# Kernel tuning notes

Measured on AMD Instinct MI355X. Metric: run time of the kernel, lower is better.

Reference implementation:

```python
import jax, jax.numpy as jnp
import numpy as np

NS, NV = 48, 10            # scalar / vector multiplicities
IN_SIZE = NS + 3*NV + 3*NV + NS   # 156
N_EDGE_FEAT = 96
HIDDEN = 96
# weight shapes per output irrep: 0e:(58,48) 1o:(68,10) 1e:(68,10) 0o:(58,48)
W_SHAPES = [('0e', NS + NV, NS), ('1o', NS + 2*NV, NV), ('1e', 2*NV + NS, NV), ('0o', NV + NS, NS)]
WEIGHT_NUMEL = sum(a*b for _, a, b in W_SHAPES)  # 6928
N_NODES, N_EDGES = 10000, 50000


def setup_inputs() -> dict:
    key = jax.random.key(0)
    ks = jax.random.split(key, 9)
    node_attr = jax.random.normal(ks[0], (N_NODES, IN_SIZE), dtype=jnp.float32)
    edge_index = jax.random.randint(ks[1], (2, N_EDGES), 0, N_NODES)
    edge_attr = jax.random.normal(ks[2], (N_EDGES, N_EDGE_FEAT), dtype=jnp.float32)
    edge_sh = jax.random.normal(ks[3], (N_EDGES, 4), dtype=jnp.float32)
    s1 = 1.0 / np.sqrt(N_EDGE_FEAT)
    s2 = 1.0 / np.sqrt(HIDDEN)
    W1 = jax.random.normal(ks[4], (N_EDGE_FEAT, HIDDEN), dtype=jnp.float32) * s1
    b1 = jnp.zeros((HIDDEN,), dtype=jnp.float32)
    W2 = jax.random.normal(ks[5], (HIDDEN, WEIGHT_NUMEL), dtype=jnp.float32) * s2
    b2 = jnp.zeros((WEIGHT_NUMEL,), dtype=jnp.float32)
    return {'node_attr': node_attr, 'edge_index': edge_index, 'edge_attr': edge_attr,
            'edge_sh': edge_sh, 'W1': W1, 'b1': b1, 'W2': W2, 'b2': b2}


def _faster_tp(in_, sh, weight):
    # in_: [E, 156], sh: [E, 4], weight: [E, 6928]
    in_0e = in_[:, :NS]                                   # [E,48]
    in_1o = in_[:, NS:NS + 3*NV].reshape(-1, NV, 3)       # [E,10,3]
    in_1e = in_[:, NS + 3*NV:NS + 6*NV].reshape(-1, NV, 3)
    in_0o = in_[:, NS + 6*NV:]                            # [E,48]
    sh_0e = sh[:, 0]                                      # [E]
    sh_1o = sh[:, 1:]                                     # [E,3]
    inv_s3 = 1.0 / np.sqrt(3.0)
    inv_s2 = 1.0 / np.sqrt(2.0)

    out_0e = jnp.concatenate([
        in_0e * sh_0e[:, None],
        jnp.sum(in_1o * sh_1o[:, None, :], axis=-1) * inv_s3], axis=-1)      # [E,58]
    out_1o = jnp.concatenate([
        in_0e[:, :, None] * sh_1o[:, None, :],
        in_1o * sh_0e[:, None, None],
        jnp.cross(in_1e, sh_1o[:, None, :]) * inv_s2], axis=-2)              # [E,68,3]
    out_1e = jnp.concatenate([
        jnp.cross(in_1o, sh_1o[:, None, :]) * inv_s2,
        in_1e * sh_0e[:, None, None],
        in_0o[:, :, None] * sh_1o[:, None, :]], axis=-2)                     # [E,68,3]
    out_0o = jnp.concatenate([
        jnp.sum(in_1e * sh_1o[:, None, :], axis=-1) * inv_s3,
        in_0o * sh_0e[:, None]], axis=-1)                                    # [E,58]

    wd = {}
    start = 0
    for name, a, b in W_SHAPES:
        wd[name] = weight[:, start:start + a*b].reshape(-1, a, b) / np.sqrt(a)
        start += a*b

    o0e = jnp.einsum('ei,eio->eo', out_0e, wd['0e'])                 # [E,48]
    o1o = jnp.einsum('eic,eio->eoc', out_1o, wd['1o']).reshape(-1, 3*NV)
    o1e = jnp.einsum('eic,eio->eoc', out_1e, wd['1e']).reshape(-1, 3*NV)
    o0o = jnp.einsum('ei,eio->eo', out_0o, wd['0o'])                 # [E,48]
    return jnp.concatenate([o0e, o1o, o1e, o0o], axis=-1)           # [E,156]


def reference(node_attr, edge_index, edge_attr, edge_sh, W1, b1, W2, b2):
    edge_src, edge_dst = edge_index[0], edge_index[1]
    # edge MLP -> per-edge TP weights
    h = jax.nn.relu(edge_attr @ W1 + b1)
    w = h @ W2 + b2                                       # [E, 6928]
    tp = _faster_tp(node_attr[edge_dst], edge_sh, w)      # [E, 156]
    # scatter-mean over source nodes
    n = node_attr.shape[0]
    seg = jax.ops.segment_sum(tp, edge_src, num_segments=n)
    cnt = jax.ops.segment_sum(jnp.ones((tp.shape[0],), tp.dtype), edge_src, num_segments=n)
    out = seg / jnp.maximum(cnt, 1.0)[:, None]
    # residual (in/out sizes equal, so pad is a no-op)
    return out + node_attr
```

## Files before the change

kernel.cpp:

```cpp
#include <hip/hip_runtime.h>

#define NE 50000
#define NN 10000
#define KH 96
#define KE 128
#define WN 6928
#define WP 7744
#define NTILE 484
#define IN_SZ 156
#define EPW 32

typedef __attribute__((ext_vector_type(8))) short short8;
typedef __attribute__((ext_vector_type(4))) float float4v;

__device__ __forceinline__ unsigned short f2bf(float x) {
  unsigned u = __float_as_uint(x);
  unsigned r = (u + 0x7FFFu + ((u >> 16) & 1u)) >> 16;
  return (unsigned short)r;
}
__device__ __forceinline__ float b2f(unsigned short u) {
  return __uint_as_float(((unsigned)u) << 16);
}

__device__ __forceinline__ void issue4(short8 (&B)[4], const unsigned short* p) {
  asm volatile("global_load_dwordx4 %0, %4, off\n\t"
               "global_load_dwordx4 %1, %4, off offset:1024\n\t"
               "global_load_dwordx4 %2, %4, off offset:2048\n\t"
               "global_load_dwordx4 %3, %4, off offset:3072"
               : "=&v"(B[0]), "=&v"(B[1]), "=&v"(B[2]), "=&v"(B[3])
               : "v"(p));
}
__device__ __forceinline__ void wait4(short8 (&B)[4]) {
  asm volatile("s_waitcnt vmcnt(4)"
               : "+v"(B[0]), "+v"(B[1]), "+v"(B[2]), "+v"(B[3]));
}
__device__ __forceinline__ void wait0(short8 (&B)[4]) {
  asm volatile("s_waitcnt vmcnt(0)"
               : "+v"(B[0]), "+v"(B[1]), "+v"(B[2]), "+v"(B[3]));
}

__global__ __launch_bounds__(256) void cast_kernel(
    const float* __restrict__ edge_attr, const float* __restrict__ W1,
    unsigned short* __restrict__ ea_bf, unsigned short* __restrict__ W1T)
{
  int idx = blockIdx.x * 256 + threadIdx.x;
  const int nea = NE * KH / 8;
  if (idx < nea) {
    const float* p = edge_attr + (size_t)idx * 8;
    float4 x = *(const float4*)p, y = *(const float4*)(p + 4);
    uint4 pk;
    pk.x = f2bf(x.x) | ((unsigned)f2bf(x.y) << 16);
    pk.y = f2bf(x.z) | ((unsigned)f2bf(x.w) << 16);
    pk.z = f2bf(y.x) | ((unsigned)f2bf(y.y) << 16);
    pk.w = f2bf(y.z) | ((unsigned)f2bf(y.w) << 16);
    *(uint4*)(ea_bf + (size_t)idx * 8) = pk;
  } else {
    int j = idx - nea;
    if (j < KH * KH) {
      int c = j / KH, k = j - c * KH;
      W1T[c * KH + k] = f2bf(W1[k * KH + c]);
    }
  }
}

__global__ __launch_bounds__(384) void mlp1_kernel(
    const unsigned short* __restrict__ ea_bf, const unsigned short* __restrict__ W1T,
    const float* __restrict__ b1, unsigned short* __restrict__ h_ext)
{
  const int tid = threadIdx.x;
  const int e0 = blockIdx.x * 16;
  const int w = tid >> 6, l = tid & 15, q = (tid >> 4) & 3;

  short8 a[3], b[3];
  #pragma unroll
  for (int s = 0; s < 3; ++s) {
    a[s] = *(const short8*)(ea_bf + (size_t)(e0 + l) * KH + s * 32 + q * 8);
    b[s] = *(const short8*)(W1T + (size_t)(w * 16 + l) * KH + s * 32 + q * 8);
  }
  float4v C = {0.f, 0.f, 0.f, 0.f};
  #pragma unroll
  for (int s = 0; s < 3; ++s)
    C = __builtin_amdgcn_mfma_f32_16x16x32_bf16(a[s], b[s], C, 0, 0, 0);

  float bv = b1[w * 16 + l];
  #pragma unroll
  for (int r = 0; r < 4; ++r)
    h_ext[(size_t)(e0 + q * 4 + r) * KE + w * 16 + l] = f2bf(fmaxf(C[r] + bv, 0.f));

  for (int idx = tid; idx < 16 * 32; idx += 384) {
    int e = idx >> 5, c = 96 + (idx & 31);
    h_ext[(size_t)(e0 + e) * KE + c] = (c == 96) ? (unsigned short)0x3F80 : (unsigned short)0;
  }
}

__global__ __launch_bounds__(256) void w2pt_kernel(
    const float* __restrict__ W2, const float* __restrict__ b2,
    unsigned short* __restrict__ W2PT)
{
  int gid = blockIdx.x * 256 + threadIdx.x;
  if (gid >= NTILE * 256) return;
  int lane = gid & 63, s = (gid >> 6) & 3, t = gid >> 8;
  int l = lane & 15, q = lane >> 4;
  int np = t * 16 + l;
  int c;
  if (np < 2784) c = np;
  else if (np < 3872) { int rel = np - 2784, i = rel >> 4, o = rel & 15; c = (o < 10) ? 2784 + i * 10 + o : -1; }
  else if (np < 4960) { int rel = np - 3872, i = rel >> 4, o = rel & 15; c = (o < 10) ? 3464 + i * 10 + o : -1; }
  else c = 4144 + (np - 4960);

  int kbase = s * 32 + q * 8;
  unsigned short o8[8];
  #pragma unroll
  for (int j = 0; j < 8; ++j) {
    int k = kbase + j;
    float v = 0.f;
    if (c >= 0) v = (k < KH) ? W2[(size_t)k * WN + c] : (k == KH ? b2[c] : 0.f);
    o8[j] = f2bf(v);
  }
  uint4 pk;
  pk.x = o8[0] | ((unsigned)o8[1] << 16);
  pk.y = o8[2] | ((unsigned)o8[3] << 16);
  pk.z = o8[4] | ((unsigned)o8[5] << 16);
  pk.w = o8[6] | ((unsigned)o8[7] << 16);
  *(uint4*)(W2PT + (size_t)gid * 8) = pk;
}

__global__ __launch_bounds__(512, 2) void tp_kernel(
    const unsigned short* __restrict__ h_ext, const float* __restrict__ node_attr,
    const int* __restrict__ edge_index, const float* __restrict__ edge_sh,
    const unsigned short* __restrict__ W2PT,
    float* __restrict__ acc, int* __restrict__ icnt)
{
  __shared__ unsigned short sIn[EPW][160];
  __shared__ float sOut[EPW][160];
  __shared__ unsigned short sF0[2][60][EPW];
  __shared__ unsigned short sF1[2][70][3][EPW];
  __shared__ float sShs[EPW][4];
  __shared__ int sSrc[EPW], sDst[EPW];

  const int tid = threadIdx.x;
  const int e0 = blockIdx.x * EPW;

  if (tid < EPW) {
    int ok = (e0 + tid) < NE;
    int s = ok ? edge_index[e0 + tid] : 0;
    int d = ok ? edge_index[NE + e0 + tid] : 0;
    sSrc[tid] = s; sDst[tid] = d;
    if (ok) atomicAdd(&icnt[s], 1);
  }
  if (tid >= 128 && tid < 256) {
    int t2 = tid - 128;
    int e = t2 >> 2, c = t2 & 3;
    sShs[e][c] = ((e0 + e) < NE) ? edge_sh[(size_t)(e0 + e) * 4 + c] : 0.f;
  }
  __syncthreads();

  for (int idx = tid; idx < EPW * IN_SZ; idx += 512) {
    int e = idx / IN_SZ, f = idx - e * IN_SZ;
    sIn[e][f] = f2bf(node_attr[(size_t)sDst[e] * IN_SZ + f]);
  }
  for (int idx = tid; idx < EPW * 160; idx += 512) (&sOut[0][0])[idx] = 0.f;
  __syncthreads();

  {
    const int e = tid >> 4, j = tid & 15;
    const float sh0 = sShs[e][0], sx = sShs[e][1], sy = sShs[e][2], sz = sShs[e][3];
    const float i3 = 0.57735026918962576f, i2 = 0.70710678118654752f;
    for (int i = j; i < 48; i += 16) {
      float v0 = b2f(sIn[e][i]), w0 = b2f(sIn[e][108 + i]);
      sF0[0][i][e] = f2bf(v0 * sh0);
      sF0[1][10 + i][e] = f2bf(w0 * sh0);
      sF1[0][i][0][e] = f2bf(v0 * sx); sF1[0][i][1][e] = f2bf(v0 * sy); sF1[0][i][2][e] = f2bf(v0 * sz);
      sF1[1][20 + i][0][e] = f2bf(w0 * sx); sF1[1][20 + i][1][e] = f2bf(w0 * sy); sF1[1][20 + i][2][e] = f2bf(w0 * sz);
    }
    if (j < 10) {
      const int v = j;
      float ax = b2f(sIn[e][48 + 3 * v]), ay = b2f(sIn[e][48 + 3 * v + 1]), az = b2f(sIn[e][48 + 3 * v + 2]);
      float bx = b2f(sIn[e][78 + 3 * v]), by = b2f(sIn[e][78 + 3 * v + 1]), bz = b2f(sIn[e][78 + 3 * v + 2]);
      sF0[0][48 + v][e] = f2bf((ax * sx + ay * sy + az * sz) * i3);
      sF0[1][v][e]      = f2bf((bx * sx + by * sy + bz * sz) * i3);
      sF1[0][48 + v][0][e] = f2bf(ax * sh0); sF1[0][48 + v][1][e] = f2bf(ay * sh0); sF1[0][48 + v][2][e] = f2bf(az * sh0);
      sF1[0][58 + v][0][e] = f2bf((by * sz - bz * sy) * i2);
      sF1[0][58 + v][1][e] = f2bf((bz * sx - bx * sz) * i2);
      sF1[0][58 + v][2][e] = f2bf((bx * sy - by * sx) * i2);
      sF1[1][v][0][e] = f2bf((ay * sz - az * sy) * i2);
      sF1[1][v][1][e] = f2bf((az * sx - ax * sz) * i2);
      sF1[1][v][2][e] = f2bf((ax * sy - ay * sx) * i2);
      sF1[1][10 + v][0][e] = f2bf(bx * sh0); sF1[1][10 + v][1][e] = f2bf(by * sh0); sF1[1][10 + v][2][e] = f2bf(bz * sh0);
    }
  }
  if (tid < 128) {
    int fam = tid >> 6, i = 58 + ((tid >> 5) & 1), e = tid & 31;
    sF0[fam][i][e] = 0;
  } else if (tid < 128 + 384) {
    int t2 = tid - 128;
    int fam = t2 / 192, r = t2 - fam * 192;
    int i = 68 + (r / 96), r2 = r % 96, cc = r2 >> 5, e = r2 & 31;
    sF1[fam][i][cc][e] = 0;
  }
  __syncthreads();

  const int wv = tid >> 6, l = tid & 15, q = (tid >> 4) & 3;

  short8 Af[2][4];
  #pragma unroll
  for (int m = 0; m < 2; ++m) {
    const unsigned short* ar = h_ext + (size_t)(e0 + m * 16 + l) * KE + q * 8;
    #pragma unroll
    for (int s = 0; s < 4; ++s) Af[m][s] = *(const short8*)(ar + s * 32);
  }

  const unsigned short* wlane = W2PT + (size_t)(tid & 63) * 8;
  short8 Ba[4], Bb[4];

  if (wv < 4) {
    const int sf = wv >> 1;
    const int ibeg = (wv & 1) * 30;
    const int tb = sf ? 310 : 0;
    const int obase = sf ? 108 : 0;
    #pragma unroll 1
    for (int ob = 0; ob < 3; ++ob) {
      float a0[4] = {0.f, 0.f, 0.f, 0.f}, a1[4] = {0.f, 0.f, 0.f, 0.f};
      auto addr = [&](int ii) {
        int i = ibeg + ii; if (i >= 58) i = ibeg;
        return wlane + (size_t)(tb + 3 * i + ob) * 2048;
      };
      auto body = [&](const short8 (&B)[4], int ii) {
        int i = ibeg + ii;
        ushort4 f0 = *(const ushort4*)&sF0[sf][i][q * 4];
        ushort4 f1 = *(const ushort4*)&sF0[sf][i][16 + q * 4];
        float4v C0 = {0.f, 0.f, 0.f, 0.f}, C1 = {0.f, 0.f, 0.f, 0.f};
        #pragma unroll
        for (int s = 0; s < 4; ++s) {
          C0 = __builtin_amdgcn_mfma_f32_16x16x32_bf16(Af[0][s], B[s], C0, 0, 0, 0);
          C1 = __builtin_amdgcn_mfma_f32_16x16x32_bf16(Af[1][s], B[s], C1, 0, 0, 0);
        }
        a0[0] += C0[0] * b2f(f0.x); a0[1] += C0[1] * b2f(f0.y);
        a0[2] += C0[2] * b2f(f0.z); a0[3] += C0[3] * b2f(f0.w);
        a1[0] += C1[0] * b2f(f1.x); a1[1] += C1[1] * b2f(f1.y);
        a1[2] += C1[2] * b2f(f1.z); a1[3] += C1[3] * b2f(f1.w);
      };
      issue4(Ba, addr(0));
      issue4(Bb, addr(1));
      #pragma unroll 1
      for (int ii = 0; ii < 28; ii += 2) {
        wait4(Ba); body(Ba, ii);     issue4(Ba, addr(ii + 2));
        wait4(Bb); body(Bb, ii + 1); issue4(Bb, addr(ii + 3));
      }
      wait4(Ba); body(Ba, 28);
      wait0(Bb); body(Bb, 29);
      const int col = obase + ob * 16 + l;
      #pragma unroll
      for (int r = 0; r < 4; ++r) {
        unsafeAtomicAdd(&sOut[q * 4 + r][col], a0[r]);
        unsafeAtomicAdd(&sOut[16 + q * 4 + r][col], a1[r]);
      }
    }
  } else {
    const int vf = (wv >> 1) - 2;
    const int ibeg = (wv & 1) ? 34 : 0;
    const int N = (wv & 1) ? 36 : 34;
    const int tb = vf ? 242 : 174;
    float r0[4][3] = {{0.f}}, r1[4][3] = {{0.f}};
    auto addr = [&](int ii) {
      int i = ibeg + ii; if (i >= 68) i = ibeg;
      return wlane + (size_t)(tb + i) * 2048;
    };
    auto body = [&](const short8 (&B)[4], int ii) {
      int i = ibeg + ii;
      ushort4 g0[3], g1[3];
      #pragma unroll
      for (int cc = 0; cc < 3; ++cc) {
        g0[cc] = *(const ushort4*)&sF1[vf][i][cc][q * 4];
        g1[cc] = *(const ushort4*)&sF1[vf][i][cc][16 + q * 4];
      }
      float4v C0 = {0.f, 0.f, 0.f, 0.f}, C1 = {0.f, 0.f, 0.f, 0.f};
      #pragma unroll
      for (int s = 0; s < 4; ++s) {
        C0 = __builtin_amdgcn_mfma_f32_16x16x32_bf16(Af[0][s], B[s], C0, 0, 0, 0);
        C1 = __builtin_amdgcn_mfma_f32_16x16x32_bf16(Af[1][s], B[s], C1, 0, 0, 0);
      }
      #pragma unroll
      for (int cc = 0; cc < 3; ++cc) {
        r0[0][cc] += C0[0] * b2f(g0[cc].x); r0[1][cc] += C0[1] * b2f(g0[cc].y);
        r0[2][cc] += C0[2] * b2f(g0[cc].z); r0[3][cc] += C0[3] * b2f(g0[cc].w);
        r1[0][cc] += C1[0] * b2f(g1[cc].x); r1[1][cc] += C1[1] * b2f(g1[cc].y);
        r1[2][cc] += C1[2] * b2f(g1[cc].z); r1[3][cc] += C1[3] * b2f(g1[cc].w);
      }
    };
    issue4(Ba, addr(0));
    issue4(Bb, addr(1));
    #pragma unroll 1
    for (int ii = 0; ii < N - 2; ii += 2) {
      wait4(Ba); body(Ba, ii);     issue4(Ba, addr(ii + 2));
      wait4(Bb); body(Bb, ii + 1); issue4(Bb, addr(ii + 3));
    }
    wait4(Ba); body(Ba, N - 2);
    wait0(Bb); body(Bb, N - 1);
    if (l < 10) {
      const int col = (vf ? 78 : 48) + 3 * l;
      #pragma unroll
      for (int r = 0; r < 4; ++r)
        #pragma unroll
        for (int cc = 0; cc < 3; ++cc) {
          unsafeAtomicAdd(&sOut[q * 4 + r][col + cc], r0[r][cc]);
          unsafeAtomicAdd(&sOut[16 + q * 4 + r][col + cc], r1[r][cc]);
        }
    }
  }
  __syncthreads();

  const float n58 = 0.13130643285972254f, n68 = 0.12126781251816650f;
  for (int idx = tid; idx < EPW * IN_SZ; idx += 512) {
    int e = idx / IN_SZ, o = idx - e * IN_SZ;
    if (e0 + e < NE) {
      float nrm = (o < 48 || o >= 108) ? n58 : n68;
      unsafeAtomicAdd(&acc[(size_t)sSrc[e] * IN_SZ + o], sOut[e][o] * nrm);
    }
  }
}

__global__ __launch_bounds__(256) void finalize_kernel(
    const float* __restrict__ acc, const int* __restrict__ icnt,
    const float* __restrict__ node_attr, float* __restrict__ out)
{
  int idx = blockIdx.x * 256 + threadIdx.x;
  if (idx < NN * IN_SZ) {
    int n = idx / IN_SZ;
    out[idx] = acc[idx] / fmaxf((float)icnt[n], 1.f) + node_attr[idx];
  }
}

extern "C" void kernel_launch(void* const* d_in, const int* in_sizes, int n_in,
                              void* d_out, int out_size, void* d_ws, size_t ws_size,
                              hipStream_t stream)
{
  const float* node_attr  = (const float*)d_in[0];
  const int*   edge_index = (const int*)d_in[1];
  const float* edge_attr  = (const float*)d_in[2];
  const float* edge_sh    = (const float*)d_in[3];
  const float* W1 = (const float*)d_in[4];
  const float* b1 = (const float*)d_in[5];
  const float* W2 = (const float*)d_in[6];
  const float* b2 = (const float*)d_in[7];
  float* out = (float*)d_out;

  unsigned short* h_ext = (unsigned short*)d_ws;
  unsigned short* W2PT  = h_ext + (size_t)50016 * KE;
  unsigned short* ea_bf = W2PT + (size_t)NTILE * 2048;
  unsigned short* W1T   = ea_bf + (size_t)NE * KH;
  float* acc  = (float*)ea_bf;
  int*   icnt = (int*)(W1T + KH * KH + 64);

  cast_kernel<<<(NE * KH / 8 + KH * KH + 255) / 256, 256, 0, stream>>>(edge_attr, W1, ea_bf, W1T);
  w2pt_kernel<<<NTILE, 256, 0, stream>>>(W2, b2, W2PT);
  mlp1_kernel<<<NE / 16, 384, 0, stream>>>(ea_bf, W1T, b1, h_ext);
  hipMemsetAsync(acc, 0, (size_t)NN * IN_SZ * sizeof(float), stream);
  hipMemsetAsync(icnt, 0, (size_t)NN * sizeof(int), stream);
  hipMemsetAsync(h_ext + (size_t)50000 * KE, 0, (size_t)16 * KE * sizeof(unsigned short), stream);
  tp_kernel<<<(NE + EPW - 1) / EPW, 512, 0, stream>>>(h_ext, node_attr, edge_index,
                                                      edge_sh, W2PT, acc, icnt);
  finalize_kernel<<<(NN * IN_SZ + 255) / 256, 256, 0, stream>>>(acc, icnt, node_attr, out);
}
```

Measured before the change: 325.4 us.

## Shrink MLP K dimension to 96, add bias in fp32, fuse edge_attr cast

Removes the bias row folded into the padded K=128 GEMM. The bias now comes from a separate fp32 vector that initializes the MFMA accumulator, so the weight stream and h_ext shrink by a quarter. The edge_attr bf16 cast is folded into the first MLP kernel, which drops a separate cast pass and its buffer. The tp_kernel uses a triple-buffered prefetch for the scalar path and raises launch bounds occupancy to 4, and the padded sF1 rows are dropped. Costs are an extra scalar load per tile and higher register pressure under the new launch bound.

```diff
diff --git a/kernel.cpp b/kernel.cpp
--- a/kernel.cpp
+++ b/kernel.cpp
@@ -3,9 +3,7 @@
 #define NE 50000
 #define NN 10000
 #define KH 96
-#define KE 128
 #define WN 6928
-#define WP 7744
 #define NTILE 484
 #define IN_SZ 156
 #define EPW 32
@@ -22,49 +20,47 @@
   return __uint_as_float(((unsigned)u) << 16);
 }
 
-__device__ __forceinline__ void issue4(short8 (&B)[4], const unsigned short* p) {
+__device__ __forceinline__ void issue3(short8 (&B)[3], float &bv,
+                                       const unsigned short* p, const float* pb) {
   asm volatile("global_load_dwordx4 %0, %4, off\n\t"
                "global_load_dwordx4 %1, %4, off offset:1024\n\t"
                "global_load_dwordx4 %2, %4, off offset:2048\n\t"
-               "global_load_dwordx4 %3, %4, off offset:3072"
-               : "=&v"(B[0]), "=&v"(B[1]), "=&v"(B[2]), "=&v"(B[3])
-               : "v"(p));
-}
-__device__ __forceinline__ void wait4(short8 (&B)[4]) {
+               "global_load_dword %3, %5, off"
+               : "=&v"(B[0]), "=&v"(B[1]), "=&v"(B[2]), "=&v"(bv)
+               : "v"(p), "v"(pb));
+}
+__device__ __forceinline__ void waitB8(short8 (&B)[3], float &bv) {
+  asm volatile("s_waitcnt vmcnt(8)"
+               : "+v"(B[0]), "+v"(B[1]), "+v"(B[2]), "+v"(bv));
+}
+__device__ __forceinline__ void waitB4(short8 (&B)[3], float &bv) {
   asm volatile("s_waitcnt vmcnt(4)"
-               : "+v"(B[0]), "+v"(B[1]), "+v"(B[2]), "+v"(B[3]));
-}
-__device__ __forceinline__ void wait0(short8 (&B)[4]) {
+               : "+v"(B[0]), "+v"(B[1]), "+v"(B[2]), "+v"(bv));
+}
+__device__ __forceinline__ void waitB0(short8 (&B)[3], float &bv) {
   asm volatile("s_waitcnt vmcnt(0)"
-               : "+v"(B[0]), "+v"(B[1]), "+v"(B[2]), "+v"(B[3]));
-}
-
-__global__ __launch_bounds__(256) void cast_kernel(
-    const float* __restrict__ edge_attr, const float* __restrict__ W1,
-    unsigned short* __restrict__ ea_bf, unsigned short* __restrict__ W1T)
-{
-  int idx = blockIdx.x * 256 + threadIdx.x;
-  const int nea = NE * KH / 8;
-  if (idx < nea) {
-    const float* p = edge_attr + (size_t)idx * 8;
-    float4 x = *(const float4*)p, y = *(const float4*)(p + 4);
-    uint4 pk;
-    pk.x = f2bf(x.x) | ((unsigned)f2bf(x.y) << 16);
-    pk.y = f2bf(x.z) | ((unsigned)f2bf(x.w) << 16);
-    pk.z = f2bf(y.x) | ((unsigned)f2bf(y.y) << 16);
-    pk.w = f2bf(y.z) | ((unsigned)f2bf(y.w) << 16);
-    *(uint4*)(ea_bf + (size_t)idx * 8) = pk;
-  } else {
-    int j = idx - nea;
-    if (j < KH * KH) {
-      int c = j / KH, k = j - c * KH;
-      W1T[c * KH + k] = f2bf(W1[k * KH + c]);
-    }
+               : "+v"(B[0]), "+v"(B[1]), "+v"(B[2]), "+v"(bv));
+}
+
+__device__ __forceinline__ int col_of_np(int np) {
+  if (np < 2784) return np;
+  if (np < 3872) { int rel = np - 2784, i = rel >> 4, o = rel & 15; return (o < 10) ? 2784 + i * 10 + o : -1; }
+  if (np < 4960) { int rel = np - 3872, i = rel >> 4, o = rel & 15; return (o < 10) ? 3464 + i * 10 + o : -1; }
+  return 4144 + (np - 4960);
+}
+
+__global__ __launch_bounds__(256) void w1t_kernel(
+    const float* __restrict__ W1, unsigned short* __restrict__ W1T)
+{
+  int j = blockIdx.x * 256 + threadIdx.x;
+  if (j < KH * KH) {
+    int c = j / KH, k = j - c * KH;
+    W1T[c * KH + k] = f2bf(W1[k * KH + c]);
   }
 }
 
 __global__ __launch_bounds__(384) void mlp1_kernel(
-    const unsigned short* __restrict__ ea_bf, const unsigned short* __restrict__ W1T,
+    const float* __restrict__ edge_attr, const unsigned short* __restrict__ W1T,
     const float* __restrict__ b1, unsigned short* __restrict__ h_ext)
 {
   const int tid = threadIdx.x;
@@ -74,7 +70,14 @@
   short8 a[3], b[3];
   #pragma unroll
   for (int s = 0; s < 3; ++s) {
-    a[s] = *(const short8*)(ea_bf + (size_t)(e0 + l) * KH + s * 32 + q * 8);
+    const float* pa = edge_attr + (size_t)(e0 + l) * KH + s * 32 + q * 8;
+    float4 x = *(const float4*)pa, y = *(const float4*)(pa + 4);
+    short8 t;
+    t[0] = (short)f2bf(x.x); t[1] = (short)f2bf(x.y);
+    t[2] = (short)f2bf(x.z); t[3] = (short)f2bf(x.w);
+    t[4] = (short)f2bf(y.x); t[5] = (short)f2bf(y.y);
+    t[6] = (short)f2bf(y.z); t[7] = (short)f2bf(y.w);
+    a[s] = t;
     b[s] = *(const short8*)(W1T + (size_t)(w * 16 + l) * KH + s * 32 + q * 8);
   }
   float4v C = {0.f, 0.f, 0.f, 0.f};
@@ -85,56 +88,51 @@
   float bv = b1[w * 16 + l];
   #pragma unroll
   for (int r = 0; r < 4; ++r)
-    h_ext[(size_t)(e0 + q * 4 + r) * KE + w * 16 + l] = f2bf(fmaxf(C[r] + bv, 0.f));
-
-  for (int idx = tid; idx < 16 * 32; idx += 384) {
-    int e = idx >> 5, c = 96 + (idx & 31);
-    h_ext[(size_t)(e0 + e) * KE + c] = (c == 96) ? (unsigned short)0x3F80 : (unsigned short)0;
-  }
+    h_ext[(size_t)(e0 + q * 4 + r) * KH + w * 16 + l] = f2bf(fmaxf(C[r] + bv, 0.f));
 }
 
 __global__ __launch_bounds__(256) void w2pt_kernel(
     const float* __restrict__ W2, const float* __restrict__ b2,
-    unsigned short* __restrict__ W2PT)
+    unsigned short* __restrict__ W2PT, float* __restrict__ b2PT)
 {
   int gid = blockIdx.x * 256 + threadIdx.x;
-  if (gid >= NTILE * 256) return;
-  int lane = gid & 63, s = (gid >> 6) & 3, t = gid >> 8;
-  int l = lane & 15, q = lane >> 4;
-  int np = t * 16 + l;
-  int c;
-  if (np < 2784) c = np;
-  else if (np < 3872) { int rel = np - 2784, i = rel >> 4, o = rel & 15; c = (o < 10) ? 2784 + i * 10 + o : -1; }
-  else if (np < 4960) { int rel = np - 3872, i = rel >> 4, o = rel & 15; c = (o < 10) ? 3464 + i * 10 + o : -1; }
-  else c = 4144 + (np - 4960);
-
-  int kbase = s * 32 + q * 8;
-  unsigned short o8[8];
-  #pragma unroll
-  for (int j = 0; j < 8; ++j) {
-    int k = kbase + j;
-    float v = 0.f;
-    if (c >= 0) v = (k < KH) ? W2[(size_t)k * WN + c] : (k == KH ? b2[c] : 0.f);
-    o8[j] = f2bf(v);
-  }
-  uint4 pk;
-  pk.x = o8[0] | ((unsigned)o8[1] << 16);
-  pk.y = o8[2] | ((unsigned)o8[3] << 16);
-  pk.z = o8[4] | ((unsigned)o8[5] << 16);
-  pk.w = o8[6] | ((unsigned)o8[7] << 16);
-  *(uint4*)(W2PT + (size_t)gid * 8) = pk;
-}
-
-__global__ __launch_bounds__(512, 2) void tp_kernel(
+  if (gid < NTILE * 192) {
+    int lane = gid & 63, s = (gid >> 6) % 3, t = gid / 192;
+    int l = lane & 15, q = lane >> 4;
+    int c = col_of_np(t * 16 + l);
+    int kbase = s * 32 + q * 8;
+    unsigned short o8[8];
+    #pragma unroll
+    for (int j = 0; j < 8; ++j) {
+      int k = kbase + j;
+      float v = (c >= 0) ? W2[(size_t)k * WN + c] : 0.f;
+      o8[j] = f2bf(v);
+    }
+    uint4 pk;
+    pk.x = o8[0] | ((unsigned)o8[1] << 16);
+    pk.y = o8[2] | ((unsigned)o8[3] << 16);
+    pk.z = o8[4] | ((unsigned)o8[5] << 16);
+    pk.w = o8[6] | ((unsigned)o8[7] << 16);
+    *(uint4*)(W2PT + (size_t)gid * 8) = pk;
+  } else {
+    int j = gid - NTILE * 192;
+    if (j < NTILE * 16) {
+      int c = col_of_np(j);
+      b2PT[j] = (c >= 0) ? b2[c] : 0.f;
+    }
+  }
+}
+
+__global__ __launch_bounds__(512, 4) void tp_kernel(
     const unsigned short* __restrict__ h_ext, const float* __restrict__ node_attr,
     const int* __restrict__ edge_index, const float* __restrict__ edge_sh,
-    const unsigned short* __restrict__ W2PT,
+    const unsigned short* __restrict__ W2PT, const float* __restrict__ b2PT,
     float* __restrict__ acc, int* __restrict__ icnt)
 {
   __shared__ unsigned short sIn[EPW][160];
-  __shared__ float sOut[EPW][160];
+  __shared__ float sOut[EPW][IN_SZ];
   __shared__ unsigned short sF0[2][60][EPW];
-  __shared__ unsigned short sF1[2][70][3][EPW];
+  __shared__ unsigned short sF1[2][68][3][EPW];
   __shared__ float sShs[EPW][4];
   __shared__ int sSrc[EPW], sDst[EPW];
 
@@ -159,7 +157,7 @@
     int e = idx / IN_SZ, f = idx - e * IN_SZ;
     sIn[e][f] = f2bf(node_attr[(size_t)sDst[e] * IN_SZ + f]);
   }
-  for (int idx = tid; idx < EPW * 160; idx += 512) (&sOut[0][0])[idx] = 0.f;
+  for (int idx = tid; idx < EPW * IN_SZ; idx += 512) (&sOut[0][0])[idx] = 0.f;
   __syncthreads();
 
   {
@@ -192,26 +190,21 @@
   if (tid < 128) {
     int fam = tid >> 6, i = 58 + ((tid >> 5) & 1), e = tid & 31;
     sF0[fam][i][e] = 0;
-  } else if (tid < 128 + 384) {
-    int t2 = tid - 128;
-    int fam = t2 / 192, r = t2 - fam * 192;
-    int i = 68 + (r / 96), r2 = r % 96, cc = r2 >> 5, e = r2 & 31;
-    sF1[fam][i][cc][e] = 0;
   }
   __syncthreads();
 
   const int wv = tid >> 6, l = tid & 15, q = (tid >> 4) & 3;
 
-  short8 Af[2][4];
+  short8 Af[2][3];
   #pragma unroll
   for (int m = 0; m < 2; ++m) {
-    const unsigned short* ar = h_ext + (size_t)(e0 + m * 16 + l) * KE + q * 8;
+    const unsigned short* ar = h_ext + (size_t)(e0 + m * 16 + l) * KH + q * 8;
     #pragma unroll
-    for (int s = 0; s < 4; ++s) Af[m][s] = *(const short8*)(ar + s * 32);
+    for (int s = 0; s < 3; ++s) Af[m][s] = *(const short8*)(ar + s * 32);
   }
 
   const unsigned short* wlane = W2PT + (size_t)(tid & 63) * 8;
-  short8 Ba[4], Bb[4];
+  const float* blane = b2PT + l;
 
   if (wv < 4) {
     const int sf = wv >> 1;
@@ -221,17 +214,19 @@
     #pragma unroll 1
     for (int ob = 0; ob < 3; ++ob) {
       float a0[4] = {0.f, 0.f, 0.f, 0.f}, a1[4] = {0.f, 0.f, 0.f, 0.f};
-      auto addr = [&](int ii) {
+      short8 Ba[3], Bb[3], Bc[3];
+      float vA, vB, vC;
+      auto taddr = [&](int ii) -> size_t {
         int i = ibeg + ii; if (i >= 58) i = ibeg;
-        return wlane + (size_t)(tb + 3 * i + ob) * 2048;
+        return (size_t)(tb + 3 * i + ob);
       };
-      auto body = [&](const short8 (&B)[4], int ii) {
+      auto body = [&](const short8 (&B)[3], float bv, int ii) {
         int i = ibeg + ii;
         ushort4 f0 = *(const ushort4*)&sF0[sf][i][q * 4];
         ushort4 f1 = *(const ushort4*)&sF0[sf][i][16 + q * 4];
-        float4v C0 = {0.f, 0.f, 0.f, 0.f}, C1 = {0.f, 0.f, 0.f, 0.f};
+        float4v C0 = {bv, bv, bv, bv}, C1 = {bv, bv, bv, bv};
         #pragma unroll
-        for (int s = 0; s < 4; ++s) {
+        for (int s = 0; s < 3; ++s) {
           C0 = __builtin_amdgcn_mfma_f32_16x16x32_bf16(Af[0][s], B[s], C0, 0, 0, 0);
           C1 = __builtin_amdgcn_mfma_f32_16x16x32_bf16(Af[1][s], B[s], C1, 0, 0, 0);
         }
@@ -240,15 +235,21 @@
         a1[0] += C1[0] * b2f(f1.x); a1[1] += C1[1] * b2f(f1.y);
         a1[2] += C1[2] * b2f(f1.z); a1[3] += C1[3] * b2f(f1.w);
       };
-      issue4(Ba, addr(0));
-      issue4(Bb, addr(1));
+      { size_t t = taddr(0); issue3(Ba, vA, wlane + t * 1536, blane + t * 16); }
+      { size_t t = taddr(1); issue3(Bb, vB, wlane + t * 1536, blane + t * 16); }
+      { size_t t = taddr(2); issue3(Bc, vC, wlane + t * 1536, blane + t * 16); }
       #pragma unroll 1
-      for (int ii = 0; ii < 28; ii += 2) {
-        wait4(Ba); body(Ba, ii);     issue4(Ba, addr(ii + 2));
-        wait4(Bb); body(Bb, ii + 1); issue4(Bb, addr(ii + 3));
-      }
-      wait4(Ba); body(Ba, 28);
-      wait0(Bb); body(Bb, 29);
+      for (int ii = 0; ii < 27; ii += 3) {
+        waitB8(Ba, vA); body(Ba, vA, ii);
+        { size_t t = taddr(ii + 3); issue3(Ba, vA, wlane + t * 1536, blane + t * 16); }
+        waitB8(Bb, vB); body(Bb, vB, ii + 1);
+        { size_t t = taddr(ii + 4); issue3(Bb, vB, wlane + t * 1536, blane + t * 16); }
+        waitB8(Bc, vC); body(Bc, vC, ii + 2);
+        { size_t t = taddr(ii + 5); issue3(Bc, vC, wlane + t * 1536, blane + t * 16); }
+      }
+      waitB8(Ba, vA); body(Ba, vA, 27);
+      waitB4(Bb, vB); body(Bb, vB, 28);
+      waitB0(Bc, vC); body(Bc, vC, 29);
       const int col = obase + ob * 16 + l;
       #pragma unroll
       for (int r = 0; r < 4; ++r) {
@@ -258,15 +259,13 @@
     }
   } else {
     const int vf = (wv >> 1) - 2;
-    const int ibeg = (wv & 1) ? 34 : 0;
-    const int N = (wv & 1) ? 36 : 34;
+    const int ibeg = (wv & 1) * 34;
     const int tb = vf ? 242 : 174;
     float r0[4][3] = {{0.f}}, r1[4][3] = {{0.f}};
-    auto addr = [&](int ii) {
-      int i = ibeg + ii; if (i >= 68) i = ibeg;
-      return wlane + (size_t)(tb + i) * 2048;
-    };
-    auto body = [&](const short8 (&B)[4], int ii) {
+    short8 Ba[3], Bb[3];
+    float vA, vB;
+    auto tadr = [&](int ii) -> size_t { return (size_t)(tb + ibeg + ii); };
+    auto body = [&](const short8 (&B)[3], float bv, int ii) {
       int i = ibeg + ii;
       ushort4 g0[3], g1[3];
       #pragma unroll
@@ -274,9 +273,9 @@
         g0[cc] = *(const ushort4*)&sF1[vf][i][cc][q * 4];
         g1[cc] = *(const ushort4*)&sF1[vf][i][cc][16 + q * 4];
       }
-      float4v C0 = {0.f, 0.f, 0.f, 0.f}, C1 = {0.f, 0.f, 0.f, 0.f};
-      #pragma unroll
-      for (int s = 0; s < 4; ++s) {
+      float4v C0 = {bv, bv, bv, bv}, C1 = {bv, bv, bv, bv};
+      #pragma unroll
+      for (int s = 0; s < 3; ++s) {
         C0 = __builtin_amdgcn_mfma_f32_16x16x32_bf16(Af[0][s], B[s], C0, 0, 0, 0);
         C1 = __builtin_amdgcn_mfma_f32_16x16x32_bf16(Af[1][s], B[s], C1, 0, 0, 0);
       }
@@ -288,15 +287,17 @@
         r1[2][cc] += C1[2] * b2f(g1[cc].z); r1[3][cc] += C1[3] * b2f(g1[cc].w);
       }
     };
-    issue4(Ba, addr(0));
-    issue4(Bb, addr(1));
+    { size_t t = tadr(0); issue3(Ba, vA, wlane + t * 1536, blane + t * 16); }
+    { size_t t = tadr(1); issue3(Bb, vB, wlane + t * 1536, blane + t * 16); }
     #pragma unroll 1
-    for (int ii = 0; ii < N - 2; ii += 2) {
-      wait4(Ba); body(Ba, ii);     issue4(Ba, addr(ii + 2));
-      wait4(Bb); body(Bb, ii + 1); issue4(Bb, addr(ii + 3));
-    }
-    wait4(Ba); body(Ba, N - 2);
-    wait0(Bb); body(Bb, N - 1);
+    for (int ii = 0; ii < 32; ii += 2) {
+      waitB4(Ba, vA); body(Ba, vA, ii);
+      { size_t t = tadr(ii + 2); issue3(Ba, vA, wlane + t * 1536, blane + t * 16); }
+      waitB4(Bb, vB); body(Bb, vB, ii + 1);
+      { size_t t = tadr(ii + 3); issue3(Bb, vB, wlane + t * 1536, blane + t * 16); }
+    }
+    waitB4(Ba, vA); body(Ba, vA, 32);
+    waitB0(Bb, vB); body(Bb, vB, 33);
     if (l < 10) {
       const int col = (vf ? 78 : 48) + 3 * l;
       #pragma unroll
@@ -346,19 +347,19 @@
   float* out = (float*)d_out;
 
   unsigned short* h_ext = (unsigned short*)d_ws;
-  unsigned short* W2PT  = h_ext + (size_t)50016 * KE;
-  unsigned short* ea_bf = W2PT + (size_t)NTILE * 2048;
-  unsigned short* W1T   = ea_bf + (size_t)NE * KH;
-  float* acc  = (float*)ea_bf;
-  int*   icnt = (int*)(W1T + KH * KH + 64);
-
-  cast_kernel<<<(NE * KH / 8 + KH * KH + 255) / 256, 256, 0, stream>>>(edge_attr, W1, ea_bf, W1T);
-  w2pt_kernel<<<NTILE, 256, 0, stream>>>(W2, b2, W2PT);
-  mlp1_kernel<<<NE / 16, 384, 0, stream>>>(ea_bf, W1T, b1, h_ext);
+  unsigned short* W2PT  = h_ext + (size_t)50016 * KH;
+  float* b2PT = (float*)(W2PT + (size_t)NTILE * 1536);
+  float* acc  = b2PT + (size_t)NTILE * 16;
+  int*   icnt = (int*)(acc + (size_t)NN * IN_SZ);
+  unsigned short* W1T = (unsigned short*)(icnt + NN);
+
+  w1t_kernel<<<(KH * KH + 255) / 256, 256, 0, stream>>>(W1, W1T);
+  w2pt_kernel<<<(NTILE * 208 + 255) / 256, 256, 0, stream>>>(W2, b2, W2PT, b2PT);
+  mlp1_kernel<<<NE / 16, 384, 0, stream>>>(edge_attr, W1T, b1, h_ext);
   hipMemsetAsync(acc, 0, (size_t)NN * IN_SZ * sizeof(float), stream);
   hipMemsetAsync(icnt, 0, (size_t)NN * sizeof(int), stream);
-  hipMemsetAsync(h_ext + (size_t)50000 * KE, 0, (size_t)16 * KE * sizeof(unsigned short), stream);
+  hipMemsetAsync(h_ext + (size_t)NE * KH, 0, (size_t)16 * KH * sizeof(unsigned short), stream);
   tp_kernel<<<(NE + EPW - 1) / EPW, 512, 0, stream>>>(h_ext, node_attr, edge_index,
-                                                      edge_sh, W2PT, acc, icnt);
+                                                      edge_sh, W2PT, b2PT, acc, icnt);
   finalize_kernel<<<(NN * IN_SZ + 255) / 256, 256, 0, stream>>>(acc, icnt, node_attr, out);
 }
```

After: 312.3 us. 4.0% less time.
